# Kernel optimization log

Measured on AMD Instinct MI355X. Metric: run time of the kernel, lower is better.

## Reference

```python
import jax, jax.numpy as jnp
import numpy as np

NUM_CLASSES = 80
NUM_TOP_QUERIES = 300


def setup_inputs() -> dict:
    key = jax.random.key(0)
    k1, k2, k3 = jax.random.split(key, 3)
    B, Q, C = 256, 1000, NUM_CLASSES
    pred_logits = jax.random.normal(k1, (B, Q, C), dtype=jnp.float32)
    pred_boxes = jax.random.uniform(k2, (B, Q, 4), dtype=jnp.float32)  # cxcywh in [0,1)
    orig_target_sizes = jax.random.uniform(k3, (B, 2), dtype=jnp.float32)  # (W, H) scale
    return {"pred_logits": pred_logits, "pred_boxes": pred_boxes,
            "orig_target_sizes": orig_target_sizes}


def _box_cxcywh_to_xyxy(boxes):
    cx, cy, w, h = jnp.split(boxes, 4, axis=-1)
    return jnp.concatenate([cx - 0.5 * w, cy - 0.5 * h, cx + 0.5 * w, cy + 0.5 * h], axis=-1)


def reference(pred_logits, pred_boxes, orig_target_sizes):
    B, Q, C = pred_logits.shape
    # cxcywh -> xyxy, then scale by [W, H, W, H]
    bbox_pred = _box_cxcywh_to_xyxy(pred_boxes)
    scale = jnp.tile(orig_target_sizes, (1, 2))[:, None, :]  # [B,1,4]
    bbox_pred = bbox_pred * scale
    # focal-loss path: sigmoid + flattened top-k over (Q*C)
    scores_all = jax.nn.sigmoid(pred_logits).reshape(B, Q * C)
    scores, index = jax.lax.top_k(scores_all, NUM_TOP_QUERIES)  # [B,K]
    labels = index % C
    q_index = index // C
    boxes = jnp.take_along_axis(bbox_pred, q_index[:, :, None], axis=1)  # [B,K,4]
    return labels, boxes, scores
```

## Files before the change

kernel.cpp:

```cpp
#include <hip/hip_runtime.h>
#include <hip/hip_bf16.h>

#define BATCH 256
#define NQ 1000
#define NC 80
#define QC 80000
#define KTOP 300
#define NT 1024
#define NBINS 4096
#define CAP 1024

__device__ __forceinline__ unsigned mono_key(float x) {
    unsigned u = __float_as_uint(x);
    return (u & 0x80000000u) ? ~u : (u | 0x80000000u);
}
__device__ __forceinline__ float inv_key(unsigned k) {
    unsigned u = (k & 0x80000000u) ? (k & 0x7FFFFFFFu) : ~k;
    return __uint_as_float(u);
}

__device__ __forceinline__ float ref_sigmoid(float x) {
    float in = __fmul_rn(0.5f, x);
    float xc = fminf(fmaxf(in, -7.90531110763549805f), 7.90531110763549805f);
    float x2 = __fmul_rn(xc, xc);
    float p = fmaf(x2, -2.76076847742355e-16f, 2.00018790482477e-13f);
    p = fmaf(x2, p, -8.60467152213735e-11f);
    p = fmaf(x2, p,  5.12229709037114e-08f);
    p = fmaf(x2, p,  1.48572235717979e-05f);
    p = fmaf(x2, p,  6.37261928875436e-04f);
    p = fmaf(x2, p,  4.89352455891786e-03f);
    float num = __fmul_rn(xc, p);
    float den = fmaf(x2, 1.19825839466702e-06f, 1.18534705686654e-04f);
    den = fmaf(x2, den, 2.26843463243900e-03f);
    den = fmaf(x2, den, 4.89352518554385e-03f);
    float t = num / den;
    t = (fabsf(in) < 0.0004f) ? in : t;
    return __fadd_rn(0.5f, __fmul_rn(0.5f, t));
}

__global__ __launch_bounds__(NT)
void rtdetr_post_kernel(const float* __restrict__ logits,
                        const float* __restrict__ boxes,
                        const float* __restrict__ sizes,
                        float* __restrict__ out) {
    __shared__ unsigned hist[NBINS];
    __shared__ unsigned long long cand[CAP];
    __shared__ unsigned scan[NT];
    __shared__ unsigned s_tbin, s_count;

    const int b = blockIdx.x;
    const int tid = threadIdx.x;
    const float4* lg4 = (const float4*)(logits + (size_t)b * QC);

    for (int i = tid; i < NBINS; i += NT) hist[i] = 0;
    if (tid == 0) s_count = 0;
    __syncthreads();

    for (int i = tid; i < QC / 4; i += NT) {
        float4 v = lg4[i];
        atomicAdd(&hist[mono_key(v.x) >> 20], 1u);
        atomicAdd(&hist[mono_key(v.y) >> 20], 1u);
        atomicAdd(&hist[mono_key(v.z) >> 20], 1u);
        atomicAdd(&hist[mono_key(v.w) >> 20], 1u);
    }
    __syncthreads();

    unsigned h0 = hist[tid * 4 + 0], h1 = hist[tid * 4 + 1];
    unsigned h2 = hist[tid * 4 + 2], h3 = hist[tid * 4 + 3];
    scan[tid] = h0 + h1 + h2 + h3;
    __syncthreads();
    for (int off = 1; off < NT; off <<= 1) {
        unsigned v = (tid + off < NT) ? scan[tid + off] : 0u;
        __syncthreads();
        scan[tid] += v;
        __syncthreads();
    }
    unsigned run = (tid + 1 < NT) ? scan[tid + 1] : 0u;
    unsigned hs[4] = {h3, h2, h1, h0};
    #pragma unroll
    for (int j = 0; j < 4; ++j) {
        unsigned bin = (unsigned)(tid * 4 + (3 - j));
        if (run < KTOP && KTOP <= run + hs[j]) s_tbin = bin;
        run += hs[j];
    }
    __syncthreads();

    unsigned thresh = s_tbin << 20;
    thresh = (thresh >= 4096u) ? thresh - 4096u : 0u;

    for (int i = tid; i < QC / 4; i += NT) {
        float4 v = lg4[i];
        float xs[4] = {v.x, v.y, v.z, v.w};
        #pragma unroll
        for (int j = 0; j < 4; ++j) {
            if (mono_key(xs[j]) >= thresh) {
                unsigned pos = atomicAdd(&s_count, 1u);
                if (pos < CAP) {
                    unsigned sk = mono_key(ref_sigmoid(xs[j]));
                    unsigned idx = (unsigned)(i * 4 + j);
                    cand[pos] = ((unsigned long long)sk << 32) | (unsigned)(~idx);
                }
            }
        }
    }
    __syncthreads();
    unsigned cnt = s_count; if (cnt > CAP) cnt = CAP;
    for (int i = tid; i < CAP; i += NT) if ((unsigned)i >= cnt) cand[i] = 0ull;
    __syncthreads();

    for (int sz = 2; sz <= CAP; sz <<= 1) {
        for (int st = sz >> 1; st > 0; st >>= 1) {
            int i = tid;
            int ixj = i ^ st;
            if (ixj > i) {
                bool desc = ((i & sz) == 0);
                unsigned long long a = cand[i], c = cand[ixj];
                bool sw = desc ? (a < c) : (a > c);
                if (sw) { cand[i] = c; cand[ixj] = a; }
            }
            __syncthreads();
        }
    }

    if (tid < KTOP) {
        unsigned long long cd = cand[tid];
        unsigned sk = (unsigned)(cd >> 32);
        unsigned idx = ~((unsigned)cd);
        float score = inv_key(sk);
        unsigned label = idx % NC;
        unsigned qi = idx / NC;
        float4 bx = ((const float4*)boxes)[(size_t)b * NQ + qi];
        float W = sizes[b * 2 + 0];
        float H = sizes[b * 2 + 1];
        float x0 = (bx.x - 0.5f * bx.z) * W;
        float y0 = (bx.y - 0.5f * bx.w) * H;
        float x1 = (bx.x + 0.5f * bx.z) * W;
        float y1 = (bx.y + 0.5f * bx.w) * H;
        int o = b * KTOP + tid;
        out[o] = (float)label;
        float* ob = out + BATCH * KTOP;
        ob[(size_t)o * 4 + 0] = x0;
        ob[(size_t)o * 4 + 1] = y0;
        ob[(size_t)o * 4 + 2] = x1;
        ob[(size_t)o * 4 + 3] = y1;
        float* os = out + BATCH * KTOP * 5;
        os[o] = score;
    }
}

extern "C" void kernel_launch(void* const* d_in, const int* in_sizes, int n_in,
                              void* d_out, int out_size, void* d_ws, size_t ws_size,
                              hipStream_t stream) {
    const float* logits = (const float*)d_in[0];
    const float* boxes  = (const float*)d_in[1];
    const float* sizes  = (const float*)d_in[2];
    float* out = (float*)d_out;
    rtdetr_post_kernel<<<BATCH, NT, 0, stream>>>(logits, boxes, sizes, out);
}
```

Before: 146.9 us.

## Speculate fixed logit threshold with histogram fallback; rank candidates by counting

The kernel first filters logits against a fixed threshold (2.55) in a single pass. It keeps the full histogram and threshold search only as a fallback for when the candidate count falls outside [KTOP, CAP]. The bitonic sort over 1024 entries is replaced with a per-thread rank count over the actual candidates, and each selected element is written directly to its output slot. This removes one full read of the logits, the histogram atomics, the scan, and the many barrier-heavy sort stages in the common case. The threshold is tuned to the expected logit distribution, so other inputs fall back to the slower two-pass path. The rank count costs O(cnt) LDS reads per thread.

```diff
diff --git a/kernel.cpp b/kernel.cpp
--- a/kernel.cpp
+++ b/kernel.cpp
@@ -9,6 +9,7 @@
 #define NT 1024
 #define NBINS 4096
 #define CAP 1024
+#define T0 2.55f
 
 __device__ __forceinline__ unsigned mono_key(float x) {
     unsigned u = __float_as_uint(x);
@@ -43,8 +44,8 @@
                         const float* __restrict__ boxes,
                         const float* __restrict__ sizes,
                         float* __restrict__ out) {
+    __shared__ unsigned long long cand[CAP];
     __shared__ unsigned hist[NBINS];
-    __shared__ unsigned long long cand[CAP];
     __shared__ unsigned scan[NT];
     __shared__ unsigned s_tbin, s_count;
 
@@ -52,48 +53,15 @@
     const int tid = threadIdx.x;
     const float4* lg4 = (const float4*)(logits + (size_t)b * QC);
 
-    for (int i = tid; i < NBINS; i += NT) hist[i] = 0;
     if (tid == 0) s_count = 0;
     __syncthreads();
-
-    for (int i = tid; i < QC / 4; i += NT) {
-        float4 v = lg4[i];
-        atomicAdd(&hist[mono_key(v.x) >> 20], 1u);
-        atomicAdd(&hist[mono_key(v.y) >> 20], 1u);
-        atomicAdd(&hist[mono_key(v.z) >> 20], 1u);
-        atomicAdd(&hist[mono_key(v.w) >> 20], 1u);
-    }
-    __syncthreads();
-
-    unsigned h0 = hist[tid * 4 + 0], h1 = hist[tid * 4 + 1];
-    unsigned h2 = hist[tid * 4 + 2], h3 = hist[tid * 4 + 3];
-    scan[tid] = h0 + h1 + h2 + h3;
-    __syncthreads();
-    for (int off = 1; off < NT; off <<= 1) {
-        unsigned v = (tid + off < NT) ? scan[tid + off] : 0u;
-        __syncthreads();
-        scan[tid] += v;
-        __syncthreads();
-    }
-    unsigned run = (tid + 1 < NT) ? scan[tid + 1] : 0u;
-    unsigned hs[4] = {h3, h2, h1, h0};
-    #pragma unroll
-    for (int j = 0; j < 4; ++j) {
-        unsigned bin = (unsigned)(tid * 4 + (3 - j));
-        if (run < KTOP && KTOP <= run + hs[j]) s_tbin = bin;
-        run += hs[j];
-    }
-    __syncthreads();
-
-    unsigned thresh = s_tbin << 20;
-    thresh = (thresh >= 4096u) ? thresh - 4096u : 0u;
 
     for (int i = tid; i < QC / 4; i += NT) {
         float4 v = lg4[i];
         float xs[4] = {v.x, v.y, v.z, v.w};
         #pragma unroll
         for (int j = 0; j < 4; ++j) {
-            if (mono_key(xs[j]) >= thresh) {
+            if (xs[j] >= T0) {
                 unsigned pos = atomicAdd(&s_count, 1u);
                 if (pos < CAP) {
                     unsigned sk = mono_key(ref_sigmoid(xs[j]));
@@ -104,47 +72,87 @@
         }
     }
     __syncthreads();
-    unsigned cnt = s_count; if (cnt > CAP) cnt = CAP;
-    for (int i = tid; i < CAP; i += NT) if ((unsigned)i >= cnt) cand[i] = 0ull;
-    __syncthreads();
+    unsigned cnt = s_count;
 
-    for (int sz = 2; sz <= CAP; sz <<= 1) {
-        for (int st = sz >> 1; st > 0; st >>= 1) {
-            int i = tid;
-            int ixj = i ^ st;
-            if (ixj > i) {
-                bool desc = ((i & sz) == 0);
-                unsigned long long a = cand[i], c = cand[ixj];
-                bool sw = desc ? (a < c) : (a > c);
-                if (sw) { cand[i] = c; cand[ixj] = a; }
-            }
+    if (cnt < KTOP || cnt > CAP) {
+        for (int i = tid; i < NBINS; i += NT) hist[i] = 0;
+        if (tid == 0) s_count = 0;
+        __syncthreads();
+        for (int i = tid; i < QC / 4; i += NT) {
+            float4 v = lg4[i];
+            atomicAdd(&hist[mono_key(v.x) >> 20], 1u);
+            atomicAdd(&hist[mono_key(v.y) >> 20], 1u);
+            atomicAdd(&hist[mono_key(v.z) >> 20], 1u);
+            atomicAdd(&hist[mono_key(v.w) >> 20], 1u);
+        }
+        __syncthreads();
+        unsigned h0 = hist[tid * 4 + 0], h1 = hist[tid * 4 + 1];
+        unsigned h2 = hist[tid * 4 + 2], h3 = hist[tid * 4 + 3];
+        scan[tid] = h0 + h1 + h2 + h3;
+        __syncthreads();
+        for (int off = 1; off < NT; off <<= 1) {
+            unsigned v = (tid + off < NT) ? scan[tid + off] : 0u;
+            __syncthreads();
+            scan[tid] += v;
             __syncthreads();
         }
+        unsigned run = (tid + 1 < NT) ? scan[tid + 1] : 0u;
+        unsigned hs[4] = {h3, h2, h1, h0};
+        #pragma unroll
+        for (int j = 0; j < 4; ++j) {
+            unsigned bin = (unsigned)(tid * 4 + (3 - j));
+            if (run < KTOP && KTOP <= run + hs[j]) s_tbin = bin;
+            run += hs[j];
+        }
+        __syncthreads();
+        unsigned thresh = s_tbin << 20;
+        thresh = (thresh >= 4096u) ? thresh - 4096u : 0u;
+        for (int i = tid; i < QC / 4; i += NT) {
+            float4 v = lg4[i];
+            float xs[4] = {v.x, v.y, v.z, v.w};
+            #pragma unroll
+            for (int j = 0; j < 4; ++j) {
+                if (mono_key(xs[j]) >= thresh) {
+                    unsigned pos = atomicAdd(&s_count, 1u);
+                    if (pos < CAP) {
+                        unsigned sk = mono_key(ref_sigmoid(xs[j]));
+                        unsigned idx = (unsigned)(i * 4 + j);
+                        cand[pos] = ((unsigned long long)sk << 32) | (unsigned)(~idx);
+                    }
+                }
+            }
+        }
+        __syncthreads();
+        cnt = s_count; if (cnt > CAP) cnt = CAP;
     }
 
-    if (tid < KTOP) {
-        unsigned long long cd = cand[tid];
-        unsigned sk = (unsigned)(cd >> 32);
-        unsigned idx = ~((unsigned)cd);
-        float score = inv_key(sk);
-        unsigned label = idx % NC;
-        unsigned qi = idx / NC;
-        float4 bx = ((const float4*)boxes)[(size_t)b * NQ + qi];
-        float W = sizes[b * 2 + 0];
-        float H = sizes[b * 2 + 1];
-        float x0 = (bx.x - 0.5f * bx.z) * W;
-        float y0 = (bx.y - 0.5f * bx.w) * H;
-        float x1 = (bx.x + 0.5f * bx.z) * W;
-        float y1 = (bx.y + 0.5f * bx.w) * H;
-        int o = b * KTOP + tid;
-        out[o] = (float)label;
-        float* ob = out + BATCH * KTOP;
-        ob[(size_t)o * 4 + 0] = x0;
-        ob[(size_t)o * 4 + 1] = y0;
-        ob[(size_t)o * 4 + 2] = x1;
-        ob[(size_t)o * 4 + 3] = y1;
-        float* os = out + BATCH * KTOP * 5;
-        os[o] = score;
+    if (tid < (int)cnt) {
+        unsigned long long my = cand[tid];
+        unsigned rank = 0;
+        for (unsigned j = 0; j < cnt; ++j) rank += (cand[j] > my) ? 1u : 0u;
+        if (rank < KTOP) {
+            unsigned sk = (unsigned)(my >> 32);
+            unsigned idx = ~((unsigned)my);
+            float score = inv_key(sk);
+            unsigned label = idx % NC;
+            unsigned qi = idx / NC;
+            float4 bx = ((const float4*)boxes)[(size_t)b * NQ + qi];
+            float W = sizes[b * 2 + 0];
+            float H = sizes[b * 2 + 1];
+            float x0 = (bx.x - 0.5f * bx.z) * W;
+            float y0 = (bx.y - 0.5f * bx.w) * H;
+            float x1 = (bx.x + 0.5f * bx.z) * W;
+            float y1 = (bx.y + 0.5f * bx.w) * H;
+            int o = b * KTOP + (int)rank;
+            out[o] = (float)label;
+            float* ob = out + BATCH * KTOP;
+            ob[(size_t)o * 4 + 0] = x0;
+            ob[(size_t)o * 4 + 1] = y0;
+            ob[(size_t)o * 4 + 2] = x1;
+            ob[(size_t)o * 4 + 3] = y1;
+            float* os = out + BATCH * KTOP * 5;
+            os[o] = score;
+        }
     }
 }
 
```

Result: faster. 128.7 us (-12.4%).
